# Performance work log

Hardware: AMD Instinct MI355X
Metric: run time of the kernel (lower is better)

## Reference

```python
import jax, jax.numpy as jnp
import numpy as np

B, S, HID = 1, 2048, 2048
NH, NKV, HD = 32, 8, 64
INTER = 8192
EPS = 1e-6


def rmsnorm(x, w, eps=EPS):
    xf = x.astype(jnp.float32)
    inv = jax.lax.rsqrt(jnp.mean(xf * xf, axis=-1, keepdims=True) + eps)
    return (xf * inv * w).astype(x.dtype)


def rope(x, sin_t, cos_t):
    # x: [B, S, H, D]; sin/cos: [S, D//2]
    sin = sin_t[None, :, None, :]
    cos = cos_t[None, :, None, :]
    d2 = x.shape[-1] // 2
    x0, x1 = x[..., :d2], x[..., d2:]
    return jnp.concatenate((x0 * cos - x1 * sin, x0 * sin + x1 * cos), axis=-1)


def setup_inputs() -> dict:
    key = jax.random.key(0)
    ks = jax.random.split(key, 12)
    hidden_states = jax.random.normal(ks[0], (B, S, HID), dtype=jnp.float32)
    # realistic RoPE tables
    inv_freq = 1.0 / (10000.0 ** (np.arange(0, HD // 2, dtype=np.float32) * 2.0 / HD))
    ang = np.arange(S, dtype=np.float32)[:, None] * inv_freq[None, :]
    sin_table = jnp.asarray(np.sin(ang))
    cos_table = jnp.asarray(np.cos(ang))
    s = 0.02
    return {
        "hidden_states": hidden_states,
        "sin_table": sin_table,
        "cos_table": cos_table,
        "ln1_w": jnp.ones((HID,), jnp.float32),
        "ln2_w": jnp.ones((HID,), jnp.float32),
        "wq": jax.random.normal(ks[1], (HID, NH * HD), jnp.float32) * s,
        "wk": jax.random.normal(ks[2], (HID, NKV * HD), jnp.float32) * s,
        "wv": jax.random.normal(ks[3], (HID, NKV * HD), jnp.float32) * s,
        "wo": jax.random.normal(ks[4], (NH * HD, HID), jnp.float32) * s,
        "w_gate": jax.random.normal(ks[5], (HID, INTER), jnp.float32) * s,
        "w_up": jax.random.normal(ks[6], (HID, INTER), jnp.float32) * s,
        "w_down": jax.random.normal(ks[7], (INTER, HID), jnp.float32) * s,
    }


def attention(x, sin_t, cos_t, wq, wk, wv, wo):
    b, s, _ = x.shape
    q = (x @ wq).reshape(b, s, NH, HD)
    k = (x @ wk).reshape(b, s, NKV, HD)
    v = (x @ wv).reshape(b, s, NKV, HD).transpose(0, 2, 1, 3)  # [B,Hk,S,D]
    q = rope(q, sin_t, cos_t).transpose(0, 2, 1, 3)  # [B,Hq,S,D]
    k = rope(k, sin_t, cos_t).transpose(0, 2, 1, 3)  # [B,Hk,S,D]
    g = NH // NKV
    k = jnp.repeat(k, g, axis=1)
    v = jnp.repeat(v, g, axis=1)
    scale = 1.0 / np.sqrt(HD)
    scores = jnp.einsum("bhqd,bhkd->bhqk", q, k) * scale
    mask = jnp.tril(jnp.ones((s, s), dtype=bool))
    scores = jnp.where(mask, scores, -jnp.inf)
    probs = jax.nn.softmax(scores, axis=-1)
    out = jnp.einsum("bhqk,bhkd->bhqd", probs, v)
    out = out.transpose(0, 2, 1, 3).reshape(b, s, NH * HD)
    return out @ wo


def reference(hidden_states, sin_table, cos_table, ln1_w, ln2_w, wq, wk, wv, wo, w_gate, w_up, w_down):
    x = hidden_states
    x = x + attention(rmsnorm(x, ln1_w), sin_table, cos_table, wq, wk, wv, wo)
    h = rmsnorm(x, ln2_w)
    x = x + (jax.nn.silu(h @ w_gate) * (h @ w_up)) @ w_down
    return x
```

## Files before the change

### kernel.cpp

```cpp
#include <hip/hip_runtime.h>
#include <hip/hip_bf16.h>

typedef float f32x4 __attribute__((ext_vector_type(4)));
typedef unsigned int u32x4 __attribute__((ext_vector_type(4)));
typedef unsigned int u32x2 __attribute__((ext_vector_type(2)));
typedef _Float16 f16x4 __attribute__((ext_vector_type(4)));
typedef unsigned short u16;

#define S_LEN 2048
#define HID 2048
#define NHEAD 32
#define NKVH 8
#define HDIM 64

__device__ __forceinline__ unsigned short f2bf_bits(float f) {
    unsigned int u = __builtin_bit_cast(unsigned int, f);
    unsigned int r = u + 0x7fffu + ((u >> 16) & 1u);
    return (unsigned short)(r >> 16);
}
__device__ __forceinline__ float bf2f(unsigned short b) {
    unsigned int u = ((unsigned int)b) << 16;
    return __builtin_bit_cast(float, u);
}
__device__ __forceinline__ unsigned cvt_pk_bf16(float lo, float hi) {
    unsigned d;
    asm("v_cvt_pk_bf16_f32 %0, %1, %2" : "=v"(d) : "v"(lo), "v"(hi));
    return d;
}

__device__ __forceinline__ f32x4 mfma_bf16(u32x4 a, u32x4 b, f32x4 c) {
    asm("v_mfma_f32_16x16x32_bf16 %0, %1, %2, %0" : "+v"(c) : "v"(a), "v"(b));
    return c;
}

__device__ __forceinline__ void gload_lds16(const void* g, void* l) {
    __builtin_amdgcn_global_load_lds(
        (const __attribute__((address_space(1))) void*)g,
        (__attribute__((address_space(3))) void*)l, 16, 0, 0);
}

__global__ __launch_bounds__(256)
void rmsnorm_k(const float* __restrict__ x, const float* __restrict__ wgt,
               unsigned short* __restrict__ out)
{
    int row = blockIdx.x;
    int t = threadIdx.x;
    const float* xr = x + (size_t)row * HID;
    f32x4 a = *(const f32x4*)(xr + t * 8);
    f32x4 b = *(const f32x4*)(xr + t * 8 + 4);
    float s = 0.f;
#pragma unroll
    for (int i = 0; i < 4; ++i) s += a[i] * a[i] + b[i] * b[i];
#pragma unroll
    for (int off = 32; off > 0; off >>= 1) s += __shfl_down(s, off);
    __shared__ float red[4];
    if ((t & 63) == 0) red[t >> 6] = s;
    __syncthreads();
    float tot = red[0] + red[1] + red[2] + red[3];
    float inv = rsqrtf(tot * (1.0f / (float)HID) + 1e-6f);
    f32x4 wa = *(const f32x4*)(wgt + t * 8);
    f32x4 wb = *(const f32x4*)(wgt + t * 8 + 4);
    unsigned int pk[4];
#pragma unroll
    for (int i = 0; i < 2; ++i) {
        pk[i]     = (unsigned)f2bf_bits(a[2*i] * inv * wa[2*i]) |
                    ((unsigned)f2bf_bits(a[2*i+1] * inv * wa[2*i+1]) << 16);
        pk[i + 2] = (unsigned)f2bf_bits(b[2*i] * inv * wb[2*i]) |
                    ((unsigned)f2bf_bits(b[2*i+1] * inv * wb[2*i+1]) << 16);
    }
    u32x4 ov; ov[0] = pk[0]; ov[1] = pk[1]; ov[2] = pk[2]; ov[3] = pk[3];
    *(u32x4*)(out + (size_t)row * HID + t * 8) = ov;
}

__global__ __launch_bounds__(256)
void transpose_cvt(const float* __restrict__ in, unsigned short* __restrict__ out,
                   int K, int N)
{
    __shared__ unsigned short tile[64 * 65];
    int kb = blockIdx.y * 64, nb = blockIdx.x * 64;
    int t = threadIdx.x;
    int r = t >> 2, c0 = (t & 3) * 16;
    const float* src = in + (size_t)(kb + r) * N + nb + c0;
#pragma unroll
    for (int j = 0; j < 4; ++j) {
        f32x4 v = *(const f32x4*)(src + j * 4);
#pragma unroll
        for (int i = 0; i < 4; ++i)
            tile[r * 65 + c0 + j * 4 + i] = f2bf_bits(v[i]);
    }
    __syncthreads();
    unsigned short e[16];
#pragma unroll
    for (int j = 0; j < 16; ++j) e[j] = tile[(c0 + j) * 65 + r];
    u32x4 o0, o1;
#pragma unroll
    for (int j = 0; j < 4; ++j) {
        o0[j] = (unsigned)e[2*j] | ((unsigned)e[2*j+1] << 16);
        o1[j] = (unsigned)e[8 + 2*j] | ((unsigned)e[8 + 2*j+1] << 16);
    }
    unsigned short* dst = out + (size_t)(nb + r) * K + kb + c0;
    *(u32x4*)(dst) = o0;
    *(u32x4*)(dst + 8) = o1;
}

__global__ __launch_bounds__(256)
void rope_k(unsigned short* __restrict__ qkv, const float* __restrict__ sin_t,
            const float* __restrict__ cos_t)
{
    int s = blockIdx.x;
    for (int it = threadIdx.x; it < (NHEAD + NKVH) * 32; it += 256) {
        int slot = it >> 5;
        int d = it & 31;
        int col = (slot < NHEAD) ? slot * 64 + d : HID + (slot - NHEAD) * 64 + d;
        unsigned short* p = qkv + (size_t)s * 3072 + col;
        float x0 = bf2f(p[0]);
        float x1 = bf2f(p[32]);
        float c = cos_t[s * 32 + d];
        float sn = sin_t[s * 32 + d];
        p[0]  = f2bf_bits(x0 * c - x1 * sn);
        p[32] = f2bf_bits(x0 * sn + x1 * c);
    }
}

__global__ __launch_bounds__(256)
void transpose_v(const unsigned short* __restrict__ qkv, unsigned short* __restrict__ vT)
{
    __shared__ unsigned short tile[64][80];
    int kb = blockIdx.x * 64, kvh = blockIdx.y;
    int t = threadIdx.x;
    int r = t >> 2, c0 = (t & 3) * 16;
    const unsigned short* src = qkv + (size_t)(kb + r) * 3072 + 2560 + kvh * 64 + c0;
    u32x4 v0 = *(const u32x4*)(src);
    u32x4 v1 = *(const u32x4*)(src + 8);
    *(u32x4*)&tile[r][c0] = v0;
    *(u32x4*)&tile[r][c0 + 8] = v1;
    __syncthreads();
    int d = t >> 2, k0 = (t & 3) * 16;
    unsigned short e[16];
#pragma unroll
    for (int j = 0; j < 16; ++j) e[j] = tile[k0 + j][d];
    u32x4 o0, o1;
#pragma unroll
    for (int j = 0; j < 4; ++j) {
        o0[j] = (unsigned)e[2*j] | ((unsigned)e[2*j+1] << 16);
        o1[j] = (unsigned)e[8 + 2*j] | ((unsigned)e[8 + 2*j+1] << 16);
    }
    int s0 = ((k0 >> 3) ^ (d & 7)) & 7;
    int s1 = (((k0 >> 3) + 1) ^ (d & 7)) & 7;
    unsigned short* dst = vT + ((size_t)kvh * 64 + d) * 2048 + kb;
    *(u32x4*)(dst + s0 * 8) = o0;
    *(u32x4*)(dst + s1 * 8) = o1;
}

template <int EPI>
__global__ __launch_bounds__(256)
void gemm_bt(const unsigned short* __restrict__ A,
             const unsigned short* __restrict__ Bt,
             void* __restrict__ outp, const void* __restrict__ auxp,
             int M, int N, int Kc, int lda)
{
    __shared__ unsigned short As[2][128 * 32];
    __shared__ unsigned short Bs[2][128 * 32];
    int t = threadIdx.x, w = t >> 6, l = t & 63;
    int rb = blockIdx.y, cb = blockIdx.x, zb = blockIdx.z;
    int wr = w >> 1, wc = w & 1;
    int l4 = l >> 4, l15 = l & 15;
    int arow = l >> 2, acol = (l & 3) * 8;
    f32x4 acc[4][4] = {};
    const unsigned short* Ag = A + (size_t)rb * 128 * lda + (size_t)zb * Kc
                                 + (size_t)(w * 16 + arow) * lda + acol;
    const unsigned short* Bg = Bt + (size_t)cb * 128 * lda + (size_t)zb * Kc
                                 + (size_t)(w * 16 + arow) * lda + acol;
    int nk = Kc >> 5;

#define STAGE(buf, kt)                                                          \
    {                                                                           \
        const unsigned short* Agk = Ag + (size_t)(kt) * 32;                     \
        const unsigned short* Bgk = Bg + (size_t)(kt) * 32;                     \
        gload_lds16(Agk, &As[buf][w * 512]);                                    \
        gload_lds16(Agk + (size_t)64 * lda, &As[buf][(4 + w) * 512]);           \
        gload_lds16(Bgk, &Bs[buf][w * 512]);                                    \
        gload_lds16(Bgk + (size_t)64 * lda, &Bs[buf][(4 + w) * 512]);           \
    }

    STAGE(0, 0);
    __syncthreads();
    int cur = 0;
    for (int kt = 0; kt < nk; ++kt) {
        if (kt + 1 < nk) STAGE(cur ^ 1, kt + 1);
        u32x4 af[4], bfr[4];
#pragma unroll
        for (int i = 0; i < 4; ++i)
            af[i] = *(const u32x4*)(&As[cur][(wr * 64 + i * 16 + l15) * 32 + l4 * 8]);
#pragma unroll
        for (int n = 0; n < 4; ++n)
            bfr[n] = *(const u32x4*)(&Bs[cur][(wc * 64 + n * 16 + l15) * 32 + l4 * 8]);
#pragma unroll
        for (int i = 0; i < 4; ++i)
#pragma unroll
            for (int n = 0; n < 4; ++n)
                acc[i][n] = mfma_bf16(af[i], bfr[n], acc[i][n]);
        __syncthreads();
        cur ^= 1;
    }
#undef STAGE

    int row0 = rb * 128 + wr * 64 + l4 * 4;
    int col0 = cb * 128 + wc * 64 + l15;
#pragma unroll
    for (int i = 0; i < 4; ++i) {
#pragma unroll
        for (int n = 0; n < 4; ++n) {
#pragma unroll
            for (int r = 0; r < 4; ++r) {
                int row = row0 + i * 16 + r;
                int col = col0 + n * 16;
                size_t idx = (size_t)row * N + col;
                float v = acc[i][n][r];
                if (EPI == 0) {
                    ((unsigned short*)outp)[idx] = f2bf_bits(v);
                } else if (EPI == 3) {
                    ((float*)outp)[idx] = v + ((const float*)auxp)[idx];
                } else {
                    ((_Float16*)outp)[(size_t)zb * M * N + idx] = (_Float16)v;
                }
            }
        }
    }
}

template <int KK>
__device__ __forceinline__ void phaseM(u16* lds, int cur, f32x4 (&acc)[8][4],
                                       int aoff, int boff,
                                       const u16* Asrc, const u16* Bsrc,
                                       int lda, int kt_stage,
                                       int dst0, int dst1)
{
    const u16* ah = lds + (cur * 4 + KK * 2) * 8192 + aoff;
    const u16* bh = lds + (cur * 4 + KK * 2 + 1) * 8192 + boff;
    u32x4 af[8], bfv[4];
    af[0] = *(const u32x4*)(ah);
#pragma unroll
    for (int ni = 0; ni < 4; ++ni) bfv[ni] = *(const u32x4*)(bh + ni * 512);
#pragma unroll
    for (int m = 1; m < 8; ++m)
        af[m] = *(const u32x4*)(ah + (m >> 2) * 2048 + (m & 3) * 512);
    {
        const u16* sa = Asrc + (size_t)kt_stage * 64 + (KK == 0 ? 32 : 0);
        const u16* sb = Bsrc + (size_t)kt_stage * 64 + (KK == 0 ? 32 : 0);
        int dbuf = (KK == 0) ? (cur ^ 1) : cur;
        u16* dA = lds + (dbuf * 4 + (KK == 0 ? 2 : 0)) * 8192;
        u16* dB = lds + (dbuf * 4 + (KK == 0 ? 3 : 1)) * 8192;
        gload_lds16(sa, dA + dst0);
        gload_lds16(sa + (size_t)128 * lda, dA + dst1);
        gload_lds16(sb, dB + dst0);
        gload_lds16(sb + (size_t)128 * lda, dB + dst1);
    }
    __builtin_amdgcn_s_barrier();
    __builtin_amdgcn_sched_barrier(0);
    __builtin_amdgcn_s_setprio(1);
#pragma unroll
    for (int m = 0; m < 8; ++m)
#pragma unroll
        for (int ni = 0; ni < 4; ++ni)
            acc[m][ni] = mfma_bf16(af[m], bfv[ni], acc[m][ni]);
    __builtin_amdgcn_s_setprio(0);
    asm volatile("s_waitcnt vmcnt(8)" ::: "memory");
    __builtin_amdgcn_s_barrier();
}

template <int EPI>
__global__ __launch_bounds__(512, 2)
void gemm8p(const u16* __restrict__ A, const u16* __restrict__ Bt,
            void* __restrict__ outp, const void* __restrict__ auxp,
            int M, int N, int Kc, int lda)
{
    extern __shared__ u16 lds[];
    const int tid = threadIdx.x;
    const int w = tid >> 6, l = tid & 63;
    const int wm = w >> 2, wn = w & 3;
    const int l4 = l >> 4, l15 = l & 15;
    const int zb = blockIdx.y;

    int wg = blockIdx.x, nwg = gridDim.x;
    int swzb = ((nwg & 7) == 0) ? ((wg & 7) * (nwg >> 3) + (wg >> 3)) : wg;
    int rbs = M >> 8;
    int rb = swzb % rbs, cb = swzb / rbs;

    const int sw = ((tid & 3) ^ ((tid >> 3) & 3)) * 8;
    const int srow = tid >> 2;
    const u16* Asrc = A + (size_t)(rb * 256 + srow) * lda + (size_t)zb * Kc + sw;
    const u16* Bsrc = Bt + (size_t)(cb * 256 + srow) * lda + (size_t)zb * Kc + sw;
    const int dst0 = tid * 8, dst1 = (512 + tid) * 8;

    const int rswz = (l15 >> 1) & 3;
    const int aoff = (wm * 128 + l15) * 32 + (l4 ^ rswz) * 8;
    const int boff = (wn * 64 + l15) * 32 + (l4 ^ rswz) * 8;

    f32x4 acc[8][4] = {};
    const int NT = Kc >> 6;

    {
#pragma unroll
        for (int h = 0; h < 2; ++h) {
            const u16* sA = Asrc + h * 32;
            const u16* sB = Bsrc + h * 32;
            gload_lds16(sA, lds + (h * 2) * 8192 + dst0);
            gload_lds16(sA + (size_t)128 * lda, lds + (h * 2) * 8192 + dst1);
            gload_lds16(sB, lds + (h * 2 + 1) * 8192 + dst0);
            gload_lds16(sB + (size_t)128 * lda, lds + (h * 2 + 1) * 8192 + dst1);
        }
        int t1 = (NT > 1) ? 1 : 0;
        const u16* sA = Asrc + (size_t)t1 * 64;
        const u16* sB = Bsrc + (size_t)t1 * 64;
        gload_lds16(sA, lds + (4 + 0) * 8192 + dst0);
        gload_lds16(sA + (size_t)128 * lda, lds + (4 + 0) * 8192 + dst1);
        gload_lds16(sB, lds + (4 + 1) * 8192 + dst0);
        gload_lds16(sB + (size_t)128 * lda, lds + (4 + 1) * 8192 + dst1);
    }
    asm volatile("s_waitcnt vmcnt(8)" ::: "memory");
    __builtin_amdgcn_s_barrier();

    for (int t = 0; t < NT; ++t) {
        int cur = t & 1;
        int k1 = (t + 1 < NT) ? t + 1 : 0;
        int k2 = (t + 2 < NT) ? t + 2 : 0;
        phaseM<0>(lds, cur, acc, aoff, boff, Asrc, Bsrc, lda, k1, dst0, dst1);
        phaseM<1>(lds, cur, acc, aoff, boff, Asrc, Bsrc, lda, k2, dst0, dst1);
    }
    asm volatile("s_waitcnt vmcnt(0)" ::: "memory");

    int row0 = rb * 256 + wm * 128 + l4 * 4;
    int col0 = cb * 256 + wn * 64 + l15;
#pragma unroll
    for (int mi = 0; mi < 8; ++mi) {
#pragma unroll
        for (int ni = 0; ni < 4; ++ni) {
#pragma unroll
            for (int r = 0; r < 4; ++r) {
                int row = row0 + mi * 16 + r;
                int col = col0 + ni * 16;
                size_t idx = (size_t)row * N + col;
                float v = acc[mi][ni][r];
                if (EPI == 1) {
                    float sv = v / (1.0f + __expf(-v));
                    ((unsigned short*)outp)[idx] = f2bf_bits(sv);
                } else if (EPI == 2) {
                    float gv = bf2f(((const unsigned short*)auxp)[idx]);
                    ((unsigned short*)outp)[idx] = f2bf_bits(v * gv);
                } else {
                    ((_Float16*)outp)[(size_t)zb * M * N + idx] = (_Float16)v;
                }
            }
        }
    }
}

template <int KK>
__device__ __forceinline__ void phaseMgu(u16* lds, int cur, f32x4 (&acc)[8][4],
                                         int aoff, int boffg, int boffu,
                                         const u16* Asrc, const u16* Bg, const u16* Bu,
                                         int lda, int kt_stage,
                                         int dst0, int dst1)
{
    const u16* ah = lds + (cur * 4 + KK * 2) * 8192 + aoff;
    const u16* bh = lds + (cur * 4 + KK * 2 + 1) * 8192;
    u32x4 af[8], bfv[4];
    af[0] = *(const u32x4*)(ah);
#pragma unroll
    for (int ni = 0; ni < 2; ++ni) {
        bfv[ni]     = *(const u32x4*)(bh + boffg + ni * 512);
        bfv[ni + 2] = *(const u32x4*)(bh + boffu + ni * 512);
    }
#pragma unroll
    for (int m = 1; m < 8; ++m)
        af[m] = *(const u32x4*)(ah + (m >> 2) * 2048 + (m & 3) * 512);
    {
        int koff = (KK == 0 ? 32 : 0);
        const u16* sa = Asrc + (size_t)kt_stage * 64 + koff;
        int dbuf = (KK == 0) ? (cur ^ 1) : cur;
        u16* dA = lds + (dbuf * 4 + (KK == 0 ? 2 : 0)) * 8192;
        u16* dB = lds + (dbuf * 4 + (KK == 0 ? 3 : 1)) * 8192;
        gload_lds16(sa, dA + dst0);
        gload_lds16(sa + (size_t)128 * lda, dA + dst1);
        gload_lds16(Bg + (size_t)kt_stage * 64 + koff, dB + dst0);
        gload_lds16(Bu + (size_t)kt_stage * 64 + koff, dB + dst1);
    }
    __builtin_amdgcn_s_barrier();
    __builtin_amdgcn_sched_barrier(0);
    __builtin_amdgcn_s_setprio(1);
#pragma unroll
    for (int m = 0; m < 8; ++m)
#pragma unroll
        for (int ni = 0; ni < 4; ++ni)
            acc[m][ni] = mfma_bf16(af[m], bfv[ni], acc[m][ni]);
    __builtin_amdgcn_s_setprio(0);
    asm volatile("s_waitcnt vmcnt(8)" ::: "memory");
    __builtin_amdgcn_s_barrier();
}

__global__ __launch_bounds__(512, 2)
void gemm8p_gu(const u16* __restrict__ A, const u16* __restrict__ WgT,
               const u16* __restrict__ WuT, unsigned short* __restrict__ outp,
               int M, int Nfull, int K)
{
    extern __shared__ u16 lds[];
    const int tid = threadIdx.x;
    const int w = tid >> 6, l = tid & 63;
    const int wm = w >> 2, wn = w & 3;
    const int l4 = l >> 4, l15 = l & 15;

    int wg = blockIdx.x, nwg = gridDim.x;
    int swzb = ((nwg & 7) == 0) ? ((wg & 7) * (nwg >> 3) + (wg >> 3)) : wg;
    int rbs = M >> 8;
    int rb = swzb % rbs, cb = swzb / rbs;

    const int sw = ((tid & 3) ^ ((tid >> 3) & 3)) * 8;
    const int srow = tid >> 2;
    const u16* Asrc = A + (size_t)(rb * 256 + srow) * K + sw;
    const u16* Bg = WgT + (size_t)(cb * 128 + srow) * K + sw;
    const u16* Bu = WuT + (size_t)(cb * 128 + srow) * K + sw;
    const int dst0 = tid * 8, dst1 = (512 + tid) * 8;

    const int rswz = (l15 >> 1) & 3;
    const int aoff  = (wm * 128 + l15) * 32 + (l4 ^ rswz) * 8;
    const int boffg = (wn * 32 + l15) * 32 + (l4 ^ rswz) * 8;
    const int boffu = (128 + wn * 32 + l15) * 32 + (l4 ^ rswz) * 8;

    f32x4 acc[8][4] = {};
    const int NT = K >> 6;

    {
#pragma unroll
        for (int h = 0; h < 2; ++h) {
            const u16* sA = Asrc + h * 32;
            gload_lds16(sA, lds + (h * 2) * 8192 + dst0);
            gload_lds16(sA + (size_t)128 * K, lds + (h * 2) * 8192 + dst1);
            gload_lds16(Bg + h * 32, lds + (h * 2 + 1) * 8192 + dst0);
            gload_lds16(Bu + h * 32, lds + (h * 2 + 1) * 8192 + dst1);
        }
        const u16* sA = Asrc + 64;
        gload_lds16(sA, lds + (4 + 0) * 8192 + dst0);
        gload_lds16(sA + (size_t)128 * K, lds + (4 + 0) * 8192 + dst1);
        gload_lds16(Bg + 64, lds + (4 + 1) * 8192 + dst0);
        gload_lds16(Bu + 64, lds + (4 + 1) * 8192 + dst1);
    }
    asm volatile("s_waitcnt vmcnt(8)" ::: "memory");
    __builtin_amdgcn_s_barrier();

    for (int t = 0; t < NT; ++t) {
        int cur = t & 1;
        int k1 = (t + 1 < NT) ? t + 1 : 0;
        int k2 = (t + 2 < NT) ? t + 2 : 0;
        phaseMgu<0>(lds, cur, acc, aoff, boffg, boffu, Asrc, Bg, Bu, K, k1, dst0, dst1);
        phaseMgu<1>(lds, cur, acc, aoff, boffg, boffu, Asrc, Bg, Bu, K, k2, dst0, dst1);
    }
    asm volatile("s_waitcnt vmcnt(0)" ::: "memory");

    int row0 = rb * 256 + wm * 128 + l4 * 4;
    int col0 = cb * 128 + wn * 32 + l15;
#pragma unroll
    for (int mi = 0; mi < 8; ++mi) {
#pragma unroll
        for (int ni = 0; ni < 2; ++ni) {
#pragma unroll
            for (int r = 0; r < 4; ++r) {
                int row = row0 + mi * 16 + r;
                int col = col0 + ni * 16;
                float gv = acc[mi][ni][r];
                float uv = acc[mi][ni + 2][r];
                float sv = gv / (1.0f + __expf(-gv)) * uv;
                outp[(size_t)row * Nfull + col] = f2bf_bits(sv);
            }
        }
    }
}

__global__ __launch_bounds__(256)
void reduce_add4(float* __restrict__ out, const _Float16* __restrict__ p, int n)
{
    int i = (blockIdx.x * 256 + threadIdx.x) * 4;
    f32x4 a = *(const f32x4*)(out + i);
#pragma unroll
    for (int z = 0; z < 4; ++z) {
        f16x4 h = *(const f16x4*)(p + (size_t)z * n + i);
#pragma unroll
        for (int j = 0; j < 4; ++j) a[j] += (float)h[j];
    }
    *(f32x4*)(out + i) = a;
}

__global__ __launch_bounds__(256)
void reduce_res4(float* __restrict__ out, const float* __restrict__ x,
                 const _Float16* __restrict__ p, int n)
{
    int i = (blockIdx.x * 256 + threadIdx.x) * 4;
    f32x4 a = *(const f32x4*)(x + i);
#pragma unroll
    for (int z = 0; z < 4; ++z) {
        f16x4 h = *(const f16x4*)(p + (size_t)z * n + i);
#pragma unroll
        for (int j = 0; j < 4; ++j) a[j] += (float)h[j];
    }
    *(f32x4*)(out + i) = a;
}

__global__ __launch_bounds__(256)
void attn_fwd(const unsigned short* __restrict__ qkv,
              const unsigned short* __restrict__ vT,
              unsigned short* __restrict__ out)
{
    int p = blockIdx.x, h = blockIdx.y, kvh = h >> 2;
    int t = threadIdx.x, w = t >> 6, l = t & 63;
    int l4 = l >> 4, l15 = l & 15;
    __shared__ unsigned short Ks[2][64 * 64];
    __shared__ unsigned short Vs[2][64 * 64];

    const unsigned short* Kg = qkv + HID + kvh * 64;
    const unsigned short* Vg = vT + (size_t)kvh * 64 * 2048;

    int ch0 = w * 2, ch1 = w * 2 + 1;
    int rsub = l >> 3;
    int ksw = ((l & 7) ^ (rsub & 7)) * 8;
    int vcol = (l & 7) * 8;
    int sw0 = (l4 ^ (l15 & 7)) * 8;
    int sw1 = ((l4 | 4) ^ (l15 & 7)) * 8;
    int srcA = ((l >> 4) & 1) * 32 + l15;
    int srcB = srcA + 16;
    bool hi32 = (l & 32) != 0;

#define STAGE_KV(buf, kt)                                                         \
    {                                                                             \
        gload_lds16(Kg + (size_t)((kt) * 64 + ch0 * 8 + rsub) * 3072 + ksw,       \
                    &Ks[buf][ch0 * 512]);                                         \
        gload_lds16(Kg + (size_t)((kt) * 64 + ch1 * 8 + rsub) * 3072 + ksw,       \
                    &Ks[buf][ch1 * 512]);                                         \
        gload_lds16(Vg + (size_t)(ch0 * 8 + rsub) * 2048 + (kt) * 64 + vcol,      \
                    &Vs[buf][ch0 * 512]);                                         \
        gload_lds16(Vg + (size_t)(ch1 * 8 + rsub) * 2048 + (kt) * 64 + vcol,      \
                    &Vs[buf][ch1 * 512]);                                         \
    }

    const float SC2 = 0.18033688f;
    const float THR = 44.36f;
    const float BIG = -3.0e38f;

    for (int half = 0; half < 2; ++half) {
        int qb = half ? (31 - p) : p;
        int qrow0 = qb * 64 + w * 16;
        STAGE_KV(0, 0);
        const unsigned short* qg = qkv + (size_t)(qrow0 + l15) * 3072 + h * 64 + l4 * 8;
        u32x4 aq0 = *(const u32x4*)(qg);
        u32x4 aq1 = *(const u32x4*)(qg + 32);
        f32x4 o[4] = {};
        float m = BIG, ls = 0.f;
        __syncthreads();
        int cur = 0;
        for (int kt = 0; kt <= qb; ++kt) {
            if (kt < qb) STAGE_KV(cur ^ 1, kt + 1);
            f32x4 sc[4];
#pragma unroll
            for (int n = 0; n < 4; ++n) {
                const unsigned short* kb_ = &Ks[cur][(n * 16 + l15) * 64];
                u32x4 b0 = *(const u32x4*)(kb_ + sw0);
                u32x4 b1 = *(const u32x4*)(kb_ + sw1);
                f32x4 z = {};
                z = mfma_bf16(b0, aq0, z);
                z = mfma_bf16(b1, aq1, z);
                sc[n] = z;
            }
            if (kt == qb) {
                int qloc = w * 16 + l15;
#pragma unroll
                for (int n = 0; n < 4; ++n)
#pragma unroll
                    for (int r = 0; r < 4; ++r)
                        if (n * 16 + l4 * 4 + r > qloc) sc[n][r] = BIG;
            }
            float rmax = BIG;
#pragma unroll
            for (int n = 0; n < 4; ++n)
#pragma unroll
                for (int r = 0; r < 4; ++r) rmax = fmaxf(rmax, sc[n][r]);
            rmax = fmaxf(rmax, __shfl_xor(rmax, 16));
            rmax = fmaxf(rmax, __shfl_xor(rmax, 32));
            if (__ballot(rmax - m > THR)) {
                float mn = fmaxf(m, rmax);
                float al = __builtin_exp2f((m - mn) * SC2);
                m = mn;
                ls *= al;
#pragma unroll
                for (int nd = 0; nd < 4; ++nd)
#pragma unroll
                    for (int r = 0; r < 4; ++r) o[nd][r] *= al;
            }
            float ms = m * SC2, rs = 0.f;
#pragma unroll
            for (int n = 0; n < 4; ++n)
#pragma unroll
                for (int r = 0; r < 4; ++r) {
                    float pe = __builtin_exp2f(__builtin_fmaf(sc[n][r], SC2, -ms));
                    sc[n][r] = pe;
                    rs += pe;
                }
            rs += __shfl_xor(rs, 16);
            rs += __shfl_xor(rs, 32);
            ls += rs;
            unsigned pk0[2], pk1[2], pk2[2], pk3[2];
#pragma unroll
            for (int rr = 0; rr < 2; ++rr) {
                pk0[rr] = cvt_pk_bf16(sc[0][2*rr], sc[0][2*rr+1]);
                pk1[rr] = cvt_pk_bf16(sc[1][2*rr], sc[1][2*rr+1]);
                pk2[rr] = cvt_pk_bf16(sc[2][2*rr], sc[2][2*rr+1]);
                pk3[rr] = cvt_pk_bf16(sc[3][2*rr], sc[3][2*rr+1]);
            }
            u32x4 W1, W2;
            {
                unsigned a0, a1;
                a0 = __shfl(pk0[0], srcA); a1 = __shfl(pk1[0], srcA); W1[0] = hi32 ? a1 : a0;
                a0 = __shfl(pk0[1], srcA); a1 = __shfl(pk1[1], srcA); W1[1] = hi32 ? a1 : a0;
                a0 = __shfl(pk0[0], srcB); a1 = __shfl(pk1[0], srcB); W1[2] = hi32 ? a1 : a0;
                a0 = __shfl(pk0[1], srcB); a1 = __shfl(pk1[1], srcB); W1[3] = hi32 ? a1 : a0;
                a0 = __shfl(pk2[0], srcA); a1 = __shfl(pk3[0], srcA); W2[0] = hi32 ? a1 : a0;
                a0 = __shfl(pk2[1], srcA); a1 = __shfl(pk3[1], srcA); W2[1] = hi32 ? a1 : a0;
                a0 = __shfl(pk2[0], srcB); a1 = __shfl(pk3[0], srcB); W2[2] = hi32 ? a1 : a0;
                a0 = __shfl(pk2[1], srcB); a1 = __shfl(pk3[1], srcB); W2[3] = hi32 ? a1 : a0;
            }
#pragma unroll
            for (int nd = 0; nd < 4; ++nd) {
                const unsigned short* vb = &Vs[cur][(nd * 16 + l15) * 64];
                u32x4 bv0 = *(const u32x4*)(vb + sw0);
                u32x4 bv1 = *(const u32x4*)(vb + sw1);
                o[nd] = mfma_bf16(bv0, W1, o[nd]);
                o[nd] = mfma_bf16(bv1, W2, o[nd]);
            }
            __syncthreads();
            cur ^= 1;
        }
#undef STAGE_KV
        float linv = 1.0f / ls;
        unsigned short* orow = out + (size_t)(qrow0 + l15) * HID + h * 64 + l4 * 4;
#pragma unroll
        for (int nd = 0; nd < 4; ++nd) {
            u32x2 wv;
            wv[0] = cvt_pk_bf16(o[nd][0] * linv, o[nd][1] * linv);
            wv[1] = cvt_pk_bf16(o[nd][2] * linv, o[nd][3] * linv);
            *(u32x2*)(orow + nd * 16) = wv;
        }
    }
}

extern "C" void kernel_launch(void* const* d_in, const int* in_sizes, int n_in,
                              void* d_out, int out_size, void* d_ws, size_t ws_size,
                              hipStream_t stream)
{
    const float* x     = (const float*)d_in[0];
    const float* sin_t = (const float*)d_in[1];
    const float* cos_t = (const float*)d_in[2];
    const float* ln1w  = (const float*)d_in[3];
    const float* ln2w  = (const float*)d_in[4];
    const float* wq    = (const float*)d_in[5];
    const float* wk    = (const float*)d_in[6];
    const float* wv    = (const float*)d_in[7];
    const float* wo    = (const float*)d_in[8];
    const float* wg    = (const float*)d_in[9];
    const float* wu    = (const float*)d_in[10];
    const float* wd    = (const float*)d_in[11];
    float* out = (float*)d_out;

    char* ws = (char*)d_ws;
    if (ws_size < 113246208u) return;
    unsigned short* wT    = (unsigned short*)(ws);
    unsigned short* xn    = (unsigned short*)(ws + 33554432u);
    unsigned short* qkv   = (unsigned short*)(ws + 41943040u);
    unsigned short* attn  = (unsigned short*)(ws + 54525952u);
    unsigned short* vT    = (unsigned short*)(ws + 62914560u);
    unsigned short* wuT   = (unsigned short*)(ws + 41943040u);
    _Float16*       part  = (_Float16*)(ws + 41943040u);
    unsigned short* g     = (unsigned short*)(ws + 79691776u);
    _Float16*       opart = (_Float16*)(ws + 79691776u);

    hipFuncSetAttribute(reinterpret_cast<const void*>(&gemm8p<5>),
                        hipFuncAttributeMaxDynamicSharedMemorySize, 131072);
    hipFuncSetAttribute(reinterpret_cast<const void*>(&gemm8p_gu),
                        hipFuncAttributeMaxDynamicSharedMemorySize, 131072);

    rmsnorm_k<<<S_LEN, 256, 0, stream>>>(x, ln1w, xn);

    transpose_cvt<<<dim3(32, 32), 256, 0, stream>>>(wq, wT, 2048, 2048);
    transpose_cvt<<<dim3(8, 32), 256, 0, stream>>>(wk, wT + (size_t)2048 * 2048, 2048, 512);
    transpose_cvt<<<dim3(8, 32), 256, 0, stream>>>(wv, wT + (size_t)2560 * 2048, 2048, 512);

    gemm_bt<0><<<dim3(24, 16, 1), 256, 0, stream>>>(xn, wT, qkv, nullptr, 2048, 3072, 2048, 2048);

    rope_k<<<S_LEN, 256, 0, stream>>>(qkv, sin_t, cos_t);
    transpose_v<<<dim3(32, 8), 256, 0, stream>>>(qkv, vT);

    attn_fwd<<<dim3(16, 32), 256, 0, stream>>>(qkv, vT, attn);

    transpose_cvt<<<dim3(32, 32), 256, 0, stream>>>(wo, wT, 2048, 2048);
    gemm8p<5><<<dim3(64, 4), 512, 131072, stream>>>(attn, wT, opart, nullptr, 2048, 2048, 512, 2048);
    reduce_res4<<<4096, 256, 0, stream>>>(out, x, opart, 4194304);

    rmsnorm_k<<<S_LEN, 256, 0, stream>>>(out, ln2w, xn);

    transpose_cvt<<<dim3(128, 32), 256, 0, stream>>>(wg, wT, 2048, 8192);
    transpose_cvt<<<dim3(128, 32), 256, 0, stream>>>(wu, wuT, 2048, 8192);
    gemm8p_gu<<<dim3(512), 512, 131072, stream>>>(xn, wT, wuT, g, 2048, 8192, 2048);

    transpose_cvt<<<dim3(32, 128), 256, 0, stream>>>(wd, wT, 8192, 2048);
    gemm8p<5><<<dim3(64, 4), 512, 131072, stream>>>(g, wT, part, nullptr, 2048, 2048, 2048, 8192);

    reduce_add4<<<4096, 256, 0, stream>>>(out, part, 4194304);
}
```

Baseline: 433.5 us.

## Double-buffer LDS fragments in registers and drop one barrier per phase

Restructures the two big GEMM main loops (gemm8p and gemm8p_gu) so that each phase loads the next half-tile's A/B fragments from LDS into a second register set while the MFMAs run on fragments loaded in the previous phase. The first fragments are preloaded before the loop, the vmcnt wait moves to the start of the phase, and the barrier between the global-to-LDS issue and the MFMA block is removed. This aims to hide LDS read latency behind matrix math and to cut synchronization. In exchange it needs 12 more 128-bit registers per thread, which risks spills under launch_bounds(512,2), and it depends on the changed wait counts still ordering async LDS writes correctly.

Result: no change. 431.5 us (-0.5%).

```diff
diff --git a/kernel.cpp b/kernel.cpp
--- a/kernel.cpp
+++ b/kernel.cpp
@@ -230,21 +230,26 @@
 }
 
 template <int KK>
-__device__ __forceinline__ void phaseM(u16* lds, int cur, f32x4 (&acc)[8][4],
+__device__ __forceinline__ void phaseP(u16* lds, int cur, f32x4 (&acc)[8][4],
+                                       u32x4 (&rcur)[12], u32x4 (&rnext)[12],
                                        int aoff, int boff,
                                        const u16* Asrc, const u16* Bsrc,
                                        int lda, int kt_stage,
                                        int dst0, int dst1)
 {
-    const u16* ah = lds + (cur * 4 + KK * 2) * 8192 + aoff;
-    const u16* bh = lds + (cur * 4 + KK * 2 + 1) * 8192 + boff;
-    u32x4 af[8], bfv[4];
-    af[0] = *(const u32x4*)(ah);
-#pragma unroll
-    for (int ni = 0; ni < 4; ++ni) bfv[ni] = *(const u32x4*)(bh + ni * 512);
-#pragma unroll
-    for (int m = 1; m < 8; ++m)
-        af[m] = *(const u32x4*)(ah + (m >> 2) * 2048 + (m & 3) * 512);
+    asm volatile("s_waitcnt vmcnt(4)" ::: "memory");
+    {
+        int nbuf = (KK == 0) ? cur : (cur ^ 1);
+        int nslot = (KK == 0) ? 2 : 0;
+        const u16* ah = lds + (nbuf * 4 + nslot) * 8192 + aoff;
+        const u16* bh = lds + (nbuf * 4 + nslot + 1) * 8192 + boff;
+#pragma unroll
+        for (int m = 0; m < 8; ++m)
+            rnext[m] = *(const u32x4*)(ah + (m >> 2) * 2048 + (m & 3) * 512);
+#pragma unroll
+        for (int ni = 0; ni < 4; ++ni)
+            rnext[8 + ni] = *(const u32x4*)(bh + ni * 512);
+    }
     {
         const u16* sa = Asrc + (size_t)kt_stage * 64 + (KK == 0 ? 32 : 0);
         const u16* sb = Bsrc + (size_t)kt_stage * 64 + (KK == 0 ? 32 : 0);
@@ -256,16 +261,14 @@
         gload_lds16(sb, dB + dst0);
         gload_lds16(sb + (size_t)128 * lda, dB + dst1);
     }
-    __builtin_amdgcn_s_barrier();
     __builtin_amdgcn_sched_barrier(0);
     __builtin_amdgcn_s_setprio(1);
 #pragma unroll
     for (int m = 0; m < 8; ++m)
 #pragma unroll
         for (int ni = 0; ni < 4; ++ni)
-            acc[m][ni] = mfma_bf16(af[m], bfv[ni], acc[m][ni]);
+            acc[m][ni] = mfma_bf16(rcur[m], rcur[8 + ni], acc[m][ni]);
     __builtin_amdgcn_s_setprio(0);
-    asm volatile("s_waitcnt vmcnt(8)" ::: "memory");
     __builtin_amdgcn_s_barrier();
 }
 
@@ -298,6 +301,7 @@
     const int boff = (wn * 64 + l15) * 32 + (l4 ^ rswz) * 8;
 
     f32x4 acc[8][4] = {};
+    u32x4 rA[12], rB[12];
     const int NT = Kc >> 6;
 
     {
@@ -320,13 +324,23 @@
     }
     asm volatile("s_waitcnt vmcnt(8)" ::: "memory");
     __builtin_amdgcn_s_barrier();
+    {
+        const u16* ah = lds + aoff;
+        const u16* bh = lds + 8192 + boff;
+#pragma unroll
+        for (int m = 0; m < 8; ++m)
+            rA[m] = *(const u32x4*)(ah + (m >> 2) * 2048 + (m & 3) * 512);
+#pragma unroll
+        for (int ni = 0; ni < 4; ++ni)
+            rA[8 + ni] = *(const u32x4*)(bh + ni * 512);
+    }
 
     for (int t = 0; t < NT; ++t) {
         int cur = t & 1;
         int k1 = (t + 1 < NT) ? t + 1 : 0;
         int k2 = (t + 2 < NT) ? t + 2 : 0;
-        phaseM<0>(lds, cur, acc, aoff, boff, Asrc, Bsrc, lda, k1, dst0, dst1);
-        phaseM<1>(lds, cur, acc, aoff, boff, Asrc, Bsrc, lda, k2, dst0, dst1);
+        phaseP<0>(lds, cur, acc, rA, rB, aoff, boff, Asrc, Bsrc, lda, k1, dst0, dst1);
+        phaseP<1>(lds, cur, acc, rB, rA, aoff, boff, Asrc, Bsrc, lda, k2, dst0, dst1);
     }
     asm volatile("s_waitcnt vmcnt(0)" ::: "memory");
 
@@ -357,24 +371,28 @@
 }
 
 template <int KK>
-__device__ __forceinline__ void phaseMgu(u16* lds, int cur, f32x4 (&acc)[8][4],
+__device__ __forceinline__ void phasePgu(u16* lds, int cur, f32x4 (&acc)[8][4],
+                                         u32x4 (&rcur)[12], u32x4 (&rnext)[12],
                                          int aoff, int boffg, int boffu,
                                          const u16* Asrc, const u16* Bg, const u16* Bu,
                                          int lda, int kt_stage,
                                          int dst0, int dst1)
 {
-    const u16* ah = lds + (cur * 4 + KK * 2) * 8192 + aoff;
-    const u16* bh = lds + (cur * 4 + KK * 2 + 1) * 8192;
-    u32x4 af[8], bfv[4];
-    af[0] = *(const u32x4*)(ah);
-#pragma unroll
-    for (int ni = 0; ni < 2; ++ni) {
-        bfv[ni]     = *(const u32x4*)(bh + boffg + ni * 512);
-        bfv[ni + 2] = *(const u32x4*)(bh + boffu + ni * 512);
-    }
-#pragma unroll
-    for (int m = 1; m < 8; ++m)
-        af[m] = *(const u32x4*)(ah + (m >> 2) * 2048 + (m & 3) * 512);
+    asm volatile("s_waitcnt vmcnt(4)" ::: "memory");
+    {
+        int nbuf = (KK == 0) ? cur : (cur ^ 1);
+        int nslot = (KK == 0) ? 2 : 0;
+        const u16* ah = lds + (nbuf * 4 + nslot) * 8192 + aoff;
+        const u16* bh = lds + (nbuf * 4 + nslot + 1) * 8192;
+#pragma unroll
+        for (int m = 0; m < 8; ++m)
+            rnext[m] = *(const u32x4*)(ah + (m >> 2) * 2048 + (m & 3) * 512);
+#pragma unroll
+        for (int ni = 0; ni < 2; ++ni) {
+            rnext[8 + ni]  = *(const u32x4*)(bh + boffg + ni * 512);
+            rnext[10 + ni] = *(const u32x4*)(bh + boffu + ni * 512);
+        }
+    }
     {
         int koff = (KK == 0 ? 32 : 0);
         const u16* sa = Asrc + (size_t)kt_stage * 64 + koff;
@@ -386,16 +404,14 @@
         gload_lds16(Bg + (size_t)kt_stage * 64 + koff, dB + dst0);
         gload_lds16(Bu + (size_t)kt_stage * 64 + koff, dB + dst1);
     }
-    __builtin_amdgcn_s_barrier();
     __builtin_amdgcn_sched_barrier(0);
     __builtin_amdgcn_s_setprio(1);
 #pragma unroll
     for (int m = 0; m < 8; ++m)
 #pragma unroll
         for (int ni = 0; ni < 4; ++ni)
-            acc[m][ni] = mfma_bf16(af[m], bfv[ni], acc[m][ni]);
+            acc[m][ni] = mfma_bf16(rcur[m], rcur[8 + ni], acc[m][ni]);
     __builtin_amdgcn_s_setprio(0);
-    asm volatile("s_waitcnt vmcnt(8)" ::: "memory");
     __builtin_amdgcn_s_barrier();
 }
 
@@ -428,6 +444,7 @@
     const int boffu = (128 + wn * 32 + l15) * 32 + (l4 ^ rswz) * 8;
 
     f32x4 acc[8][4] = {};
+    u32x4 rA[12], rB[12];
     const int NT = K >> 6;
 
     {
@@ -447,13 +464,25 @@
     }
     asm volatile("s_waitcnt vmcnt(8)" ::: "memory");
     __builtin_amdgcn_s_barrier();
+    {
+        const u16* ah = lds + aoff;
+        const u16* bh = lds + 8192;
+#pragma unroll
+        for (int m = 0; m < 8; ++m)
+            rA[m] = *(const u32x4*)(ah + (m >> 2) * 2048 + (m & 3) * 512);
+#pragma unroll
+        for (int ni = 0; ni < 2; ++ni) {
+            rA[8 + ni]  = *(const u32x4*)(bh + boffg + ni * 512);
+            rA[10 + ni] = *(const u32x4*)(bh + boffu + ni * 512);
+        }
+    }
 
     for (int t = 0; t < NT; ++t) {
         int cur = t & 1;
         int k1 = (t + 1 < NT) ? t + 1 : 0;
         int k2 = (t + 2 < NT) ? t + 2 : 0;
-        phaseMgu<0>(lds, cur, acc, aoff, boffg, boffu, Asrc, Bg, Bu, K, k1, dst0, dst1);
-        phaseMgu<1>(lds, cur, acc, aoff, boffg, boffu, Asrc, Bg, Bu, K, k2, dst0, dst1);
+        phasePgu<0>(lds, cur, acc, rA, rB, aoff, boffg, boffu, Asrc, Bg, Bu, K, k1, dst0, dst1);
+        phasePgu<1>(lds, cur, acc, rB, rA, aoff, boffg, boffu, Asrc, Bg, Bu, K, k2, dst0, dst1);
     }
     asm volatile("s_waitcnt vmcnt(0)" ::: "memory");
 
```
